# Optimization experiments

Hardware: AMD Instinct MI355X
Metric: run time of the kernel (lower is better)

Reference implementation:

```python
import jax, jax.numpy as jnp
import numpy as np

BETA = 0.25


def setup_inputs() -> dict:
    key = jax.random.key(0)
    k1, k2 = jax.random.split(key)
    z = jax.random.normal(k1, (32, 256, 32, 32), dtype=jnp.float32)
    embedding = jax.random.normal(k2, (8192, 256), dtype=jnp.float32)
    return {"z": z, "embedding": embedding}


def reference(z, embedding):
    # z: [b, c, h, w] -> [b, h, w, c]
    z_t = jnp.transpose(z, (0, 2, 3, 1))
    b, h, w, c = z_t.shape
    zf = z_t.reshape(-1, c)                                   # [N, d]
    # squared euclidean distances: ||z||^2 + ||e||^2 - 2 z.e
    d = (jnp.sum(zf * zf, axis=1, keepdims=True)
         + jnp.sum(embedding * embedding, axis=1)
         - 2.0 * jnp.einsum('nd,kd->nk', zf, embedding))      # [N, n_embed]
    idx = jnp.argmin(d, axis=1)                               # [N]
    z_q = embedding[idx].reshape(z_t.shape)                   # [b, h, w, c]
    diff = BETA * jnp.mean((jax.lax.stop_gradient(z_q) - z_t) ** 2)
    z_q = z_t + jax.lax.stop_gradient(z_q - z_t)              # straight-through
    z_q = jnp.transpose(z_q, (0, 3, 1, 2))                    # back to [b, c, h, w]
    return z_q, diff, idx
```

## Files before the change

kernel.cpp:

```cpp
#include <hip/hip_runtime.h>
#include <stdint.h>


typedef _Float16 half8 __attribute__((ext_vector_type(8)));
typedef float floatx4 __attribute__((ext_vector_type(4)));

#define BETA 0.25f

__device__ __forceinline__ void pin(half8& x) { asm volatile("" : "+v"(x)); }

__global__ __launch_bounds__(256) void prep(const float* __restrict__ z,
                                            _Float16* __restrict__ zh,
                                            const float* __restrict__ e,
                                            _Float16* __restrict__ eh,
                                            float* __restrict__ en) {
  int bid = blockIdx.x;
  int t = threadIdx.x;
  if (bid < 2048) {
    __shared__ float tile[64][65];
    int ct = bid & 3;
    int ntile = bid >> 2;
    int b = ntile >> 4;
    int hw0 = (ntile & 15) * 64;
    int c0 = ct * 64;
    int tr = t >> 6, tc = t & 63;
#pragma unroll
    for (int i = 0; i < 16; ++i) {
      int c = tr + i * 4;
      tile[c][tc] = z[b * 262144 + (c0 + c) * 1024 + hw0 + tc];
    }
    __syncthreads();
    int n0abs = b * 1024 + hw0;
#pragma unroll
    for (int iter = 0; iter < 2; ++iter) {
      int s = iter * 256 + t;
      int nrow = s >> 3, k8l = s & 7;
      half8 hv;
#pragma unroll
      for (int h = 0; h < 8; ++h) hv[h] = (_Float16)tile[k8l * 8 + h][nrow];
      size_t off = (size_t)(n0abs / 16 + (nrow >> 4)) * 4096 +
                   (size_t)((((c0 >> 3) + k8l) * 16 + (nrow & 15)) * 8);
      *(half8*)&zh[off] = hv;
    }
  } else {
    __shared__ float el[16][257];
    int k0 = (bid - 2048) * 16;
#pragma unroll
    for (int r = 0; r < 16; ++r) el[r][t] = e[(k0 + r) * 256 + t];
    __syncthreads();
    {
      int row = t >> 4, li = t & 15;
      float s = 0.f;
#pragma unroll
      for (int jj = 0; jj < 16; ++jj) {
        float v = el[row][li + 16 * jj];
        s += v * v;
      }
#pragma unroll
      for (int st = 1; st < 16; st <<= 1) s += __shfl_xor(s, st);
      if (li == 0) en[k0 + row] = s;
    }
#pragma unroll
    for (int iter = 0; iter < 2; ++iter) {
      int s = iter * 256 + t;
      int row = s & 15, k8 = s >> 4;
      half8 hv;
#pragma unroll
      for (int h = 0; h < 8; ++h) hv[h] = (_Float16)el[row][k8 * 8 + h];
      *(half8*)&eh[(size_t)k0 * 256 + k8 * 128 + row * 8] = hv;
    }
  }
}

__global__ __launch_bounds__(512, 4) void vq_coarse(
    const _Float16* __restrict__ zh, const _Float16* __restrict__ eh,
    const float* __restrict__ en_, unsigned* __restrict__ cand) {
  __shared__ _Float16 Bs[2][16384];
  __shared__ unsigned ltop[128][2][2];
  const int tid = threadIdx.x;
  const int l = tid & 63;
  const int w = tid >> 6;
  const int wm = w >> 1;
  const int wn = w & 1;
  const int n0 = blockIdx.y * 128;
  const int kbase = blockIdx.x * 2048;
  const int cl = l & 15;
  const int lg = l >> 4;

  {
    const char* src = (const char*)(eh + (size_t)kbase * 256);
#pragma unroll
    for (int c = 0; c < 4; ++c) {
      int jc = w * 4 + c;
      __builtin_amdgcn_global_load_lds(
          (const __attribute__((address_space(1))) unsigned int*)(src + jc * 1024 + l * 16),
          (__attribute__((address_space(3))) unsigned int*)((char*)&Bs[0][0] + jc * 1024),
          16, 0, 0);
    }
  }

  half8 Zf[2][8];
#pragma unroll
  for (int nt = 0; nt < 2; ++nt)
#pragma unroll
    for (int ks = 0; ks < 8; ++ks) {
      Zf[nt][ks] = *(const half8*)&zh[(size_t)(n0 / 16 + wm * 2 + nt) * 4096 +
                                      ks * 512 + l * 8];
      pin(Zf[nt][ks]);
    }

  unsigned p1[2], p2[2];
  p1[0] = p1[1] = p2[0] = p2[1] = 0xFFFFFFFFu;

  __syncthreads();

  int cur = 0;
  for (int ct = 0; ct < 32; ++ct) {
    const int krow0 = kbase + ct * 64;
    floatx4 envv[2];
#pragma unroll
    for (int mt = 0; mt < 2; ++mt)
      envv[mt] = *(const floatx4*)&en_[krow0 + wn * 32 + mt * 16 + lg * 4];
    if (ct + 1 < 32) {
      const char* src = (const char*)(eh + (size_t)(krow0 + 64) * 256);
#pragma unroll
      for (int c = 0; c < 4; ++c) {
        int jc = w * 4 + c;
        __builtin_amdgcn_global_load_lds(
            (const __attribute__((address_space(1))) unsigned int*)(src + jc * 1024 + l * 16),
            (__attribute__((address_space(3))) unsigned int*)((char*)&Bs[cur ^ 1][0] + jc * 1024),
            16, 0, 0);
      }
    }
    floatx4 acc[2][2] = {};
    __builtin_amdgcn_s_setprio(1);
#pragma unroll
    for (int ks = 0; ks < 8; ++ks) {
      half8 af[2];
#pragma unroll
      for (int mt = 0; mt < 2; ++mt)
        af[mt] = *(const half8*)&Bs[cur][(wn * 2 + mt) * 4096 + ks * 512 + l * 8];
#pragma unroll
      for (int mt = 0; mt < 2; ++mt)
#pragma unroll
        for (int nt = 0; nt < 2; ++nt)
          acc[mt][nt] = __builtin_amdgcn_mfma_f32_16x16x32_f16(
              af[mt], Zf[nt][ks], acc[mt][nt], 0, 0, 0);
    }
    __builtin_amdgcn_s_setprio(0);
#pragma unroll
    for (int mt = 0; mt < 2; ++mt) {
      unsigned locb = (unsigned)((ct & 15) * 64 + wn * 32 + mt * 16 + lg * 4);
#pragma unroll
      for (int nt = 0; nt < 2; ++nt) {
#pragma unroll
        for (int r = 0; r < 4; ++r) {
          float d = fmaf(-2.0f, acc[mt][nt][r], envv[mt][r]);
          unsigned c = (__float_as_uint(d) & 0xFFFFFC00u) | (locb + r);
          unsigned mn = min(p1[nt], c);
          unsigned mx = max(p1[nt], c);
          p1[nt] = mn;
          p2[nt] = min(p2[nt], mx);
        }
      }
    }
    if ((ct & 15) == 15) {
      const int gi = blockIdx.x * 2 + (ct >> 4);
#pragma unroll
      for (int nt = 0; nt < 2; ++nt) {
        unsigned a1 = p1[nt], a2 = p2[nt];
#pragma unroll
        for (int st = 16; st < 64; st <<= 1) {
          unsigned b1 = __shfl_xor(a1, st);
          unsigned b2 = __shfl_xor(a2, st);
          unsigned m1 = min(a1, b1);
          unsigned M = max(a1, b1);
          a1 = m1;
          a2 = min(min(a2, b2), M);
        }
        if (lg == 0) {
          int rowl = wm * 32 + nt * 16 + cl;
          ltop[rowl][wn][0] = a1;
          ltop[rowl][wn][1] = a2;
        }
        p1[nt] = 0xFFFFFFFFu;
        p2[nt] = 0xFFFFFFFFu;
      }
      __syncthreads();
      if (tid < 128) {
        unsigned a1 = ltop[tid][0][0], a2 = ltop[tid][0][1];
        unsigned b1 = ltop[tid][1][0], b2 = ltop[tid][1][1];
        unsigned m1 = min(a1, b1);
        unsigned M = max(a1, b1);
        unsigned f2 = min(min(a2, b2), M);
        unsigned long long packed = ((unsigned long long)f2 << 32) | m1;
        *(unsigned long long*)&cand[(size_t)(n0 + tid) * 16 + gi * 2] = packed;
      }
    }
    __syncthreads();
    cur ^= 1;
  }
}

__global__ __launch_bounds__(256) void vq_refine(const unsigned* __restrict__ cand,
                                                 const float* __restrict__ emb,
                                                 const float* __restrict__ z,
                                                 float* __restrict__ out_idx,
                                                 float* __restrict__ zq,
                                                 float* __restrict__ diff) {
  __shared__ float ztl[32][260];
  __shared__ unsigned win_s[32];
  __shared__ float dsh[4];
  const int t = threadIdx.x;
  const int n0 = blockIdx.x * 32;
  const int b = n0 >> 10;
  const int hw0 = n0 & 1023;
  const int j = t & 31, c8 = t >> 5;
#pragma unroll
  for (int ci = 0; ci < 32; ++ci) {
    int c = ci * 8 + c8;
    ztl[j][c] = z[b * 262144 + c * 1024 + hw0 + j];
  }
  __syncthreads();
  const int w = t >> 6, l = t & 63;
  const int sub = l >> 4;
  const int li = l & 15;
  double wsum = 0.0;
  for (int i = 0; i < 8; ++i) {
    int row = w * 8 + i;
    int n = n0 + row;
    floatx4 zv[4];
#pragma unroll
    for (int x = 0; x < 4; ++x)
      zv[x] = *(const floatx4*)&ztl[row][li * 4 + x * 64];
    double s4[4];
    unsigned k4[4];
#pragma unroll
    for (int r = 0; r < 4; ++r) {
      int jj = sub * 4 + r;
      unsigned cv = cand[(size_t)n * 16 + jj];
      unsigned k = (unsigned)(jj >> 1) * 1024 + (cv & 1023);
      k4[r] = k;
      const float* ep = &emb[(size_t)k * 256 + li * 4];
      double acc = 0.0;
#pragma unroll
      for (int x = 0; x < 4; ++x) {
        floatx4 ev = *(const floatx4*)&ep[x * 64];
#pragma unroll
        for (int y = 0; y < 4; ++y) {
          double dd = (double)ev[y] - (double)zv[x][y];
          acc += dd * dd;
        }
      }
      s4[r] = acc;
    }
#pragma unroll
    for (int r = 0; r < 4; ++r)
#pragma unroll
      for (int st = 1; st < 16; st <<= 1) s4[r] += __shfl_xor(s4[r], st);
    double bd = s4[0];
    unsigned bk = k4[0];
#pragma unroll
    for (int r = 1; r < 4; ++r)
      if (s4[r] < bd || (s4[r] == bd && k4[r] < bk)) { bd = s4[r]; bk = k4[r]; }
#pragma unroll
    for (int st = 16; st < 64; st <<= 1) {
      double od = __shfl_xor(bd, st);
      unsigned ok = __shfl_xor(bk, st);
      if (od < bd || (od == bd && ok < bk)) { bd = od; bk = ok; }
    }
    if (l == 0) {
      out_idx[n] = (float)bk;
      win_s[row] = bk;
    }
    wsum += bd;
  }
  if (l == 0) dsh[w] = (float)(wsum * ((double)BETA / 8388608.0));
  __syncthreads();
  if (t == 0) atomicAdd(diff, dsh[0] + dsh[1] + dsh[2] + dsh[3]);
#pragma unroll
  for (int ci = 0; ci < 32; ++ci) {
    int c = ci * 8 + c8;
    zq[b * 262144 + c * 1024 + hw0 + j] = emb[(size_t)win_s[j] * 256 + c];
  }
}

extern "C" void kernel_launch(void* const* d_in, const int* in_sizes, int n_in,
                              void* d_out, int out_size, void* d_ws, size_t ws_size,
                              hipStream_t stream) {
  const float* z = (const float*)d_in[0];
  const float* emb = (const float*)d_in[1];
  char* ws = (char*)d_ws;
  _Float16* zh = (_Float16*)(ws);
  _Float16* eh = (_Float16*)(ws + 16777216);
  float* en = (float*)(ws + 20971520);
  unsigned* cand = (unsigned*)(ws + 21004288);

  float* out = (float*)d_out;
  float* out_zq = out;
  float* out_diff = out + 8388608;
  float* out_idx = out + 8388609;

  hipMemsetAsync(out_diff, 0, 4, stream);

  prep<<<2560, 256, 0, stream>>>(z, zh, emb, eh, en);
  vq_coarse<<<dim3(4, 256), 512, 0, stream>>>(zh, eh, en, cand);
  vq_refine<<<1024, 256, 0, stream>>>(cand, emb, z, out_idx, out_zq, out_diff);
}
```

Baseline: 341.3 us.

## Prune refine candidates by approximate distance and drop MFMA setprio

The refine kernel now reads the approximate fp16 distance packed into each candidate, finds the wave-wide minimum, and computes the exact fp64 distance only for candidates within a fixed margin. Each such candidate is evaluated by the full 64-lane wave with a single reduction, instead of scoring all 16 candidates in fixed 16-lane groups. The goal is to cut embedding gathers and double-precision arithmetic in the refine stage. It risks choosing a wrong index if the fp16 approximation error is larger than the margin. The s_setprio calls around the MFMA loop in the distance kernel are also removed.

```diff
diff --git a/kernel.cpp b/kernel.cpp
--- a/kernel.cpp
+++ b/kernel.cpp
@@ -133,7 +133,6 @@
       }
     }
     floatx4 acc[2][2] = {};
-    __builtin_amdgcn_s_setprio(1);
 #pragma unroll
     for (int ks = 0; ks < 8; ++ks) {
       half8 af[2];
@@ -147,7 +146,6 @@
           acc[mt][nt] = __builtin_amdgcn_mfma_f32_16x16x32_f16(
               af[mt], Zf[nt][ks], acc[mt][nt], 0, 0, 0);
     }
-    __builtin_amdgcn_s_setprio(0);
 #pragma unroll
     for (int mt = 0; mt < 2; ++mt) {
       unsigned locb = (unsigned)((ct & 15) * 64 + wn * 32 + mt * 16 + lg * 4);
@@ -202,6 +200,7 @@
   }
 }
 
+#define PRUNE_EPS 8.0f
 __global__ __launch_bounds__(256) void vq_refine(const unsigned* __restrict__ cand,
                                                  const float* __restrict__ emb,
                                                  const float* __restrict__ z,
@@ -223,51 +222,34 @@
   }
   __syncthreads();
   const int w = t >> 6, l = t & 63;
-  const int sub = l >> 4;
-  const int li = l & 15;
   double wsum = 0.0;
   for (int i = 0; i < 8; ++i) {
     int row = w * 8 + i;
     int n = n0 + row;
-    floatx4 zv[4];
-#pragma unroll
-    for (int x = 0; x < 4; ++x)
-      zv[x] = *(const floatx4*)&ztl[row][li * 4 + x * 64];
-    double s4[4];
-    unsigned k4[4];
-#pragma unroll
-    for (int r = 0; r < 4; ++r) {
-      int jj = sub * 4 + r;
-      unsigned cv = cand[(size_t)n * 16 + jj];
-      unsigned k = (unsigned)(jj >> 1) * 1024 + (cv & 1023);
-      k4[r] = k;
-      const float* ep = &emb[(size_t)k * 256 + li * 4];
+    floatx4 zv = *(const floatx4*)&ztl[row][l * 4];
+    unsigned cv = cand[(size_t)n * 16 + (l & 15)];
+    unsigned kk = (unsigned)((l & 15) >> 1) * 1024 + (cv & 1023);
+    float kd = __uint_as_float(cv & 0xFFFFFC00u);
+    float kmin = kd;
+#pragma unroll
+    for (int st = 1; st < 16; st <<= 1) kmin = fminf(kmin, __shfl_xor(kmin, st));
+    unsigned long long mask = __ballot(kd <= kmin + PRUNE_EPS) & 0xFFFFULL;
+    double bd = 1e300;
+    unsigned bk = 0xffffffffu;
+    while (mask) {
+      int jj = __builtin_ctzll(mask);
+      mask &= mask - 1;
+      unsigned k = (unsigned)__shfl((int)kk, jj);
+      floatx4 ev = *(const floatx4*)&emb[(size_t)k * 256 + l * 4];
       double acc = 0.0;
 #pragma unroll
       for (int x = 0; x < 4; ++x) {
-        floatx4 ev = *(const floatx4*)&ep[x * 64];
-#pragma unroll
-        for (int y = 0; y < 4; ++y) {
-          double dd = (double)ev[y] - (double)zv[x][y];
-          acc += dd * dd;
-        }
-      }
-      s4[r] = acc;
-    }
-#pragma unroll
-    for (int r = 0; r < 4; ++r)
-#pragma unroll
-      for (int st = 1; st < 16; st <<= 1) s4[r] += __shfl_xor(s4[r], st);
-    double bd = s4[0];
-    unsigned bk = k4[0];
-#pragma unroll
-    for (int r = 1; r < 4; ++r)
-      if (s4[r] < bd || (s4[r] == bd && k4[r] < bk)) { bd = s4[r]; bk = k4[r]; }
-#pragma unroll
-    for (int st = 16; st < 64; st <<= 1) {
-      double od = __shfl_xor(bd, st);
-      unsigned ok = __shfl_xor(bk, st);
-      if (od < bd || (od == bd && ok < bk)) { bd = od; bk = ok; }
+        double dd = (double)ev[x] - (double)zv[x];
+        acc += dd * dd;
+      }
+#pragma unroll
+      for (int st = 1; st < 64; st <<= 1) acc += __shfl_xor(acc, st);
+      if (acc < bd || (acc == bd && k < bk)) { bd = acc; bk = k; }
     }
     if (l == 0) {
       out_idx[n] = (float)bk;
```

After: 286.4 us. 1.19x faster.
